# Kernel optimization log

Measured on AMD Instinct MI355X. Metric: run time of the kernel, lower is better.

## Reference

```python
import jax, jax.numpy as jnp
import numpy as np

N_NODES = 100000
N_EDGES = 1600000
C_IN = 128
C_OUT = 128


def setup_inputs() -> dict:
    key = jax.random.key(0)
    k1, k2, k3, k4, k5 = jax.random.split(key, 5)
    x = jax.random.normal(k1, (N_NODES, C_IN), dtype=jnp.float32)
    W = jax.random.normal(k2, (2 * C_IN, C_OUT), dtype=jnp.float32) * (1.0 / np.sqrt(2 * C_IN))
    b = jax.random.normal(k3, (C_OUT,), dtype=jnp.float32) * 0.01
    src = jax.random.randint(k4, (N_EDGES,), 0, N_NODES, dtype=jnp.int64 if jax.config.jax_enable_x64 else jnp.int32)
    dst = jax.random.randint(k5, (N_EDGES,), 0, N_NODES, dtype=jnp.int64 if jax.config.jax_enable_x64 else jnp.int32)
    return {"x": x, "W": W, "b": b, "src": src, "dst": dst}


def reference(x, W, b, src, dst):
    # Max-Relative graph conv: per-edge relative feature, max-aggregated per dst node.
    diff = x[dst] - x[src]                                  # [E, C]  (edge messages)
    max_diff = jax.ops.segment_max(diff, dst, num_segments=x.shape[0])  # [N, C]
    # Nodes with no incoming edges: segment_max yields -inf; zero them out.
    max_diff = jnp.where(jnp.isneginf(max_diff), jnp.zeros_like(max_diff), max_diff)
    h = jnp.concatenate([x, max_diff], axis=1)              # [N, 2C]
    return jax.nn.relu(h @ W + b)                           # Linear(2C->C_out) + ReLU
```

## Files before the change

### kernel.cpp

```cpp
#include <hip/hip_runtime.h>
#include <math.h>

#define NN 100000
#define NE 1600000
#define C 128

#define TS 4096
#define NT ((NE + TS - 1) / TS)
#define BUK ((NN + 511) >> 9)
#define NSC (BUK * NT)
#define NBS ((NSC + 2047) / 2048)
#define PREP_BLKS (NN * C / 8 / 256)
#define CONVW_BLKS (2 * C * C / 256)
#define GM 64

typedef __attribute__((ext_vector_type(8))) short   bf16x8;
typedef __attribute__((ext_vector_type(4))) float   f32x4;
typedef unsigned short ushort_t;
typedef unsigned int   uint_t;

__device__ inline ushort_t f2bf(float f) {
    union { float f; uint_t u; } a; a.f = f;
    uint_t r = a.u + 0x7fff + ((a.u >> 16) & 1);
    return (ushort_t)(r >> 16);
}

__global__ __launch_bounds__(256) void k_setup(
        const float* __restrict__ x, ushort_t* __restrict__ xh,
        const float* __restrict__ W, ushort_t* __restrict__ Wt,
        const int* __restrict__ dst, int* __restrict__ tileHistT) {
    __shared__ int h[BUK];
    const int t  = threadIdx.x;
    const int bb = blockIdx.x;
    if (bb < PREP_BLKS) {
        int i = bb * 256 + t;
        int node = i >> 4;
        int c0   = (i & 15) * 8;
        const float4* xp = (const float4*)(x + (long)i * 8);
        float4 v0 = xp[0], v1 = xp[1];
        ushort_t o[8] = { f2bf(v0.x), f2bf(v0.y), f2bf(v0.z), f2bf(v0.w),
                          f2bf(v1.x), f2bf(v1.y), f2bf(v1.z), f2bf(v1.w) };
        *(bf16x8*)(xh + (long)node * 256 + c0) = *(bf16x8*)o;
    } else if (bb < PREP_BLKS + CONVW_BLKS) {
        int i = (bb - PREP_BLKS) * 256 + t;
        int k = i >> 7, n = i & 127;
        Wt[n * 256 + k] = f2bf(W[i]);
    } else {
        const int tile = bb - PREP_BLKS - CONVW_BLKS;
        for (int i = t; i < BUK; i += 256) h[i] = 0;
        __syncthreads();
        const int base = tile * TS;
        for (int i = t; i < TS; i += 256) {
            int e = base + i;
            if (e < NE) atomicAdd(&h[dst[e] >> 9], 1);
        }
        __syncthreads();
        for (int i = t; i < BUK; i += 256) tileHistT[i * NT + tile] = h[i];
    }
}

__global__ __launch_bounds__(256) void scan_partial(const int* __restrict__ in,
                                                    int* __restrict__ out,
                                                    int* __restrict__ blocksums,
                                                    int n) {
    __shared__ int ts[256];
    const int t = threadIdx.x;
    const int base = blockIdx.x * 2048 + t * 8;
    int c[8];
    int s = 0;
    #pragma unroll
    for (int j = 0; j < 8; ++j) {
        int i = base + j;
        c[j] = (i < n) ? in[i] : 0;
        s += c[j];
    }
    ts[t] = s;
    __syncthreads();
    for (int off = 1; off < 256; off <<= 1) {
        int add = (t >= off) ? ts[t - off] : 0;
        __syncthreads();
        ts[t] += add;
        __syncthreads();
    }
    int run = (t == 0) ? 0 : ts[t - 1];
    #pragma unroll
    for (int j = 0; j < 8; ++j) {
        int i = base + j;
        if (i < n) out[i] = run;
        run += c[j];
    }
    if (t == 255) blocksums[blockIdx.x] = ts[255];
}

__global__ __launch_bounds__(64) void scan_blocksums(const int* __restrict__ blocksums,
                                                     int* __restrict__ blockbase, int nb) {
    int lane = threadIdx.x;
    int v = (lane < nb) ? blocksums[lane] : 0;
    int incl = v;
    #pragma unroll
    for (int off = 1; off < 64; off <<= 1) {
        int nbr = __shfl_up(incl, off, 64);
        if (lane >= off) incl += nbr;
    }
    if (lane < nb) blockbase[lane] = incl - v;
}

__global__ __launch_bounds__(256) void p3_scatter(const int* __restrict__ dst,
                                                  const int* __restrict__ src,
                                                  const int* __restrict__ tileScan,
                                                  const int* __restrict__ blockbase,
                                                  uint_t* __restrict__ coarse) {
    __shared__ int cur[BUK];
    const int t = threadIdx.x, tile = blockIdx.x;
    for (int i = t; i < BUK; i += 256) {
        int idx = i * NT + tile;
        cur[i] = tileScan[idx] + blockbase[idx >> 11];
    }
    __syncthreads();
    const int base = tile * TS;
    for (int i = t; i < TS; i += 256) {
        int e = base + i;
        if (e < NE) {
            int d = dst[e];
            int p = atomicAdd(&cur[d >> 9], 1);
            coarse[p] = ((uint_t)(d & 511) << 17) | (uint_t)src[e];
        }
    }
}

__global__ __launch_bounds__(256) void p4_build(const uint_t* __restrict__ coarse,
                                                const int* __restrict__ tileScan,
                                                const int* __restrict__ blockbase,
                                                int* __restrict__ offs,
                                                int* __restrict__ ssrc) {
    __shared__ int cnt[512];
    __shared__ int ts[256];
    const int b = blockIdx.x, t = threadIdx.x;
    const int n0 = b << 9;
    const int i0 = b * NT;
    const int bs = tileScan[i0] + blockbase[i0 >> 11];
    int be;
    if (b == BUK - 1) be = NE;
    else { int i1 = (b + 1) * NT; be = tileScan[i1] + blockbase[i1 >> 11]; }
    cnt[t] = 0; cnt[t + 256] = 0;
    __syncthreads();
    for (int i = bs + t; i < be; i += 256)
        atomicAdd(&cnt[(int)(coarse[i] >> 17)], 1);
    __syncthreads();
    int c0 = cnt[2 * t], c1 = cnt[2 * t + 1];
    ts[t] = c0 + c1;
    __syncthreads();
    for (int off = 1; off < 256; off <<= 1) {
        int add = (t >= off) ? ts[t - off] : 0;
        __syncthreads();
        ts[t] += add;
        __syncthreads();
    }
    int ex = (t == 0) ? 0 : ts[t - 1];
    int o0 = bs + ex, o1 = o0 + c0;
    cnt[2 * t] = o0; cnt[2 * t + 1] = o1;
    if (n0 + 2 * t < NN)     offs[n0 + 2 * t]     = o0;
    if (n0 + 2 * t + 1 < NN) offs[n0 + 2 * t + 1] = o1;
    if (b == BUK - 1 && t == 0) offs[NN] = NE;
    __syncthreads();
    for (int i = bs + t; i < be; i += 256) {
        uint_t pk = coarse[i];
        int p = atomicAdd(&cnt[(int)(pk >> 17)], 1);
        ssrc[p] = (int)(pk & 0x1FFFF);
    }
}

#define ACCQ(u)  { m[0] = fminf(m[0], __uint_as_float((u).x << 16));          \
                   m[1] = fminf(m[1], __uint_as_float((u).x & 0xffff0000u));  \
                   m[2] = fminf(m[2], __uint_as_float((u).y << 16));          \
                   m[3] = fminf(m[3], __uint_as_float((u).y & 0xffff0000u));  \
                   m[4] = fminf(m[4], __uint_as_float((u).z << 16));          \
                   m[5] = fminf(m[5], __uint_as_float((u).z & 0xffff0000u));  \
                   m[6] = fminf(m[6], __uint_as_float((u).w << 16));          \
                   m[7] = fminf(m[7], __uint_as_float((u).w & 0xffff0000u)); }

__global__ __launch_bounds__(256) void node_min_v2(
        const int* __restrict__ offs, const int* __restrict__ ssrc,
        ushort_t* __restrict__ xh) {
    const int wid  = (blockIdx.x * 256 + threadIdx.x) >> 6;
    const int lane = threadIdx.x & 63;
    if (wid >= NN) return;
    const int g = lane >> 4;
    const int s = lane & 15;
    const int beg = offs[wid], end = offs[wid + 1];
    const char* xb = (const char*)xh;
    float m[8];
    #pragma unroll
    for (int j = 0; j < 8; ++j) m[j] = INFINITY;
    int i = beg;
    for (; i + 8 <= end; i += 8) {
        int e0 = ssrc[i + g];
        int e1 = ssrc[i + 4 + g];
        uint4 a = *(const uint4*)(xb + (long)e0 * 512 + s * 16);
        uint4 bq = *(const uint4*)(xb + (long)e1 * 512 + s * 16);
        ACCQ(a);
        ACCQ(bq);
    }
    for (; i < end; i += 4) {
        int e = i + g;
        int idx = ssrc[(e < end) ? e : (end - 1)];
        uint4 a = *(const uint4*)(xb + (long)idx * 512 + s * 16);
        if (e < end) ACCQ(a);
    }
    #pragma unroll
    for (int j = 0; j < 8; ++j) {
        m[j] = fminf(m[j], __shfl_xor(m[j], 16, 64));
        m[j] = fminf(m[j], __shfl_xor(m[j], 32, 64));
    }
    if (g == 0) {
        uint4 xd = *(const uint4*)(xb + (long)wid * 512 + s * 16);
        uint_t xu[4] = { xd.x, xd.y, xd.z, xd.w };
        bool has = end > beg;
        uint4 o;
        uint_t* op = (uint_t*)&o;
        #pragma unroll
        for (int j = 0; j < 4; ++j) {
            float lo = has ? (__uint_as_float(xu[j] << 16)         - m[2 * j])     : 0.0f;
            float hi = has ? (__uint_as_float(xu[j] & 0xffff0000u) - m[2 * j + 1]) : 0.0f;
            op[j] = (uint_t)f2bf(lo) | ((uint_t)f2bf(hi) << 16);
        }
        *(uint4*)((char*)xh + (long)wid * 512 + 256 + s * 16) = o;
    }
}

__global__ __launch_bounds__(256) void gemm_mfma(
        const ushort_t* __restrict__ xh, const ushort_t* __restrict__ Wt,
        const float* __restrict__ b, float* __restrict__ out) {
    const int w    = threadIdx.x >> 6;
    const int l    = threadIdx.x & 63;
    const int wcol = w * 32;
    const int lr   = l & 15;
    const int kb   = (l >> 4) * 8;

    bf16x8 bb[2][8];
    float  bv[2];
    #pragma unroll
    for (int n = 0; n < 2; ++n) {
        int col = wcol + n * 16 + lr;
        bv[n] = b[col];
        const ushort_t* wp = Wt + (long)col * 256 + kb;
        #pragma unroll
        for (int k0 = 0; k0 < 8; ++k0)
            bb[n][k0] = *(const bf16x8*)(wp + k0 * 32);
    }

    const int mb0 = blockIdx.x * GM;
    #pragma unroll
    for (int mt = 0; mt < GM / 16; ++mt) {
        int mbase = mb0 + mt * 16;
        int arow = mbase + lr;
        if (arow >= NN) arow = NN - 1;
        const ushort_t* ap = xh + (long)arow * 256 + kb;
        bf16x8 a[8];
        #pragma unroll
        for (int k0 = 0; k0 < 8; ++k0) a[k0] = *(const bf16x8*)(ap + k0 * 32);

        f32x4 acc0 = (f32x4){0.f, 0.f, 0.f, 0.f};
        f32x4 acc1 = (f32x4){0.f, 0.f, 0.f, 0.f};
        #pragma unroll
        for (int k0 = 0; k0 < 8; ++k0) {
            acc0 = __builtin_amdgcn_mfma_f32_16x16x32_bf16(a[k0], bb[0][k0], acc0, 0, 0, 0);
            acc1 = __builtin_amdgcn_mfma_f32_16x16x32_bf16(a[k0], bb[1][k0], acc1, 0, 0, 0);
        }

        int rbase = mbase + ((l >> 4) << 2);
        int col0 = wcol + lr;
        #pragma unroll
        for (int j = 0; j < 4; ++j) {
            int r = rbase + j;
            if (r < NN) {
                out[(long)r * 128 + col0]      = fmaxf(acc0[j] + bv[0], 0.0f);
                out[(long)r * 128 + col0 + 16] = fmaxf(acc1[j] + bv[1], 0.0f);
            }
        }
    }
}

__global__ void init_neginf(float* __restrict__ p, int n) {
    int i = blockIdx.x * blockDim.x + threadIdx.x;
    if (i < n) p[i] = -INFINITY;
}

__device__ inline void amaxf(float* a, float v, float cur) {
    if (cur >= v) return;
    if (v >= 0.0f) atomicMax((int*)a, __float_as_int(v));
    else           atomicMin((unsigned int*)a, __float_as_uint(v));
}

__global__ __launch_bounds__(256) void edge_max(
        const float* __restrict__ x, const int* __restrict__ src,
        const int* __restrict__ dst, float* __restrict__ maxdiff) {
    long tid = (long)blockIdx.x * blockDim.x + threadIdx.x;
    int e = (int)(tid >> 5);
    if (e >= NE) return;
    int lane = (int)(tid & 31);
    int s = src[e], d = dst[e];
    int c0 = lane * 4;
    const float4 xd = *(const float4*)(x + (long)d * C + c0);
    const float4 xs = *(const float4*)(x + (long)s * C + c0);
    float4 df;
    df.x = xd.x - xs.x; df.y = xd.y - xs.y;
    df.z = xd.z - xs.z; df.w = xd.w - xs.w;
    float* o = maxdiff + (long)d * C + c0;
    float4 cur = *(const float4*)o;
    amaxf(o + 0, df.x, cur.x);
    amaxf(o + 1, df.y, cur.y);
    amaxf(o + 2, df.z, cur.z);
    amaxf(o + 3, df.w, cur.w);
}

#define TN 32
__global__ __launch_bounds__(256) void gemm_relu(
        const float* __restrict__ x, const float* __restrict__ W,
        const float* __restrict__ b, float* __restrict__ out) {
    __shared__ float h[TN][2 * C];
    const int nb = blockIdx.x * TN;
    const int t  = threadIdx.x;
    for (int i = t; i < TN * 2 * C / 4; i += 256) {
        int idx  = i * 4;
        int node = idx / (2 * C);
        int ci   = idx % (2 * C);
        float4 v;
        if (ci < C) {
            v = *(const float4*)(x + (long)(nb + node) * C + ci);
        } else {
            v = *(const float4*)(out + (long)(nb + node) * C + (ci - C));
            if (v.x == -INFINITY) v.x = 0.0f;
            if (v.y == -INFINITY) v.y = 0.0f;
            if (v.z == -INFINITY) v.z = 0.0f;
            if (v.w == -INFINITY) v.w = 0.0f;
        }
        *(float4*)&h[node][ci] = v;
    }
    __syncthreads();
    const int co = (t & 31) * 4;
    const int n0 = (t >> 5) * 4;
    float acc[4][4];
    #pragma unroll
    for (int i = 0; i < 4; ++i)
        #pragma unroll
        for (int j = 0; j < 4; ++j) acc[i][j] = 0.0f;
    for (int ci = 0; ci < 2 * C; ++ci) {
        float4 w = *(const float4*)(W + (long)ci * C + co);
        #pragma unroll
        for (int i = 0; i < 4; ++i) {
            float hv = h[n0 + i][ci];
            acc[i][0] = fmaf(hv, w.x, acc[i][0]);
            acc[i][1] = fmaf(hv, w.y, acc[i][1]);
            acc[i][2] = fmaf(hv, w.z, acc[i][2]);
            acc[i][3] = fmaf(hv, w.w, acc[i][3]);
        }
    }
    float4 bias = *(const float4*)(b + co);
    #pragma unroll
    for (int i = 0; i < 4; ++i) {
        float4 r;
        r.x = fmaxf(acc[i][0] + bias.x, 0.0f);
        r.y = fmaxf(acc[i][1] + bias.y, 0.0f);
        r.z = fmaxf(acc[i][2] + bias.z, 0.0f);
        r.w = fmaxf(acc[i][3] + bias.w, 0.0f);
        *(float4*)(out + (long)(nb + n0 + i) * C + co) = r;
    }
}

extern "C" void kernel_launch(void* const* d_in, const int* in_sizes, int n_in,
                              void* d_out, int out_size, void* d_ws, size_t ws_size,
                              hipStream_t stream) {
    const float* x   = (const float*)d_in[0];
    const float* W   = (const float*)d_in[1];
    const float* b   = (const float*)d_in[2];
    const int*   src = (const int*)d_in[3];
    const int*   dst = (const int*)d_in[4];
    float* out = (float*)d_out;

    size_t ints_head = (size_t)128 + NSC + (NN + 1) + NE;
    size_t head_b    = ((ints_head * 4) + 255) & ~(size_t)255;
    size_t xh_b      = (size_t)NN * 256 * 2;
    size_t wt_b      = (size_t)2 * C * C * 2;
    size_t need      = head_b + xh_b + wt_b;

    if (ws_size >= need) {
        int* blocksums = (int*)d_ws;
        int* blockbase = blocksums + 64;
        int* tileScan  = blockbase + 64;
        int* offs      = tileScan + NSC;
        int* ssrc      = offs + NN + 1;
        ushort_t* xh   = (ushort_t*)((char*)d_ws + head_b);
        ushort_t* Wt   = (ushort_t*)((char*)d_ws + head_b + xh_b);
        int*    tileHistT = ssrc;
        uint_t* coarse    = (uint_t*)d_out;

        k_setup<<<PREP_BLKS + CONVW_BLKS + NT, 256, 0, stream>>>(x, xh, W, Wt, dst, tileHistT);
        scan_partial<<<NBS, 256, 0, stream>>>(tileHistT, tileScan, blocksums, NSC);
        scan_blocksums<<<1, 64, 0, stream>>>(blocksums, blockbase, NBS);
        p3_scatter<<<NT, 256, 0, stream>>>(dst, src, tileScan, blockbase, coarse);
        p4_build<<<BUK, 256, 0, stream>>>(coarse, tileScan, blockbase, offs, ssrc);
        node_min_v2<<<NN / 4, 256, 0, stream>>>(offs, ssrc, xh);
        gemm_mfma<<<(NN + GM - 1) / GM, 256, 0, stream>>>(xh, Wt, b, out);
    } else {
        int n = NN * C;
        init_neginf<<<(n + 255) / 256, 256, 0, stream>>>(out, n);
        long threads = (long)NE * 32;
        edge_max<<<(int)((threads + 255) / 256), 256, 0, stream>>>(x, src, dst, out);
        gemm_relu<<<(NN + TN - 1) / TN, 256, 0, stream>>>(x, W, b, out);
    }
}
```

Before: 269.4 us.

## Gather order-preserving bf16 keys for packed u16 min, fold blocksum scan into consumers

Result: no change. 272.0 us (+1.0%).

```diff
diff --git a/kernel.cpp b/kernel.cpp
--- a/kernel.cpp
+++ b/kernel.cpp
@@ -14,8 +14,9 @@
 #define CONVW_BLKS (2 * C * C / 256)
 #define GM 64
 
-typedef __attribute__((ext_vector_type(8))) short   bf16x8;
-typedef __attribute__((ext_vector_type(4))) float   f32x4;
+typedef __attribute__((ext_vector_type(8))) short          bf16x8;
+typedef __attribute__((ext_vector_type(4))) float          f32x4;
+typedef __attribute__((ext_vector_type(8))) unsigned short u16x8;
 typedef unsigned short ushort_t;
 typedef unsigned int   uint_t;
 
@@ -27,6 +28,7 @@
 
 __global__ __launch_bounds__(256) void k_setup(
         const float* __restrict__ x, ushort_t* __restrict__ xh,
+        ushort_t* __restrict__ xt,
         const float* __restrict__ W, ushort_t* __restrict__ Wt,
         const int* __restrict__ dst, int* __restrict__ tileHistT) {
     __shared__ int h[BUK];
@@ -40,7 +42,12 @@
         float4 v0 = xp[0], v1 = xp[1];
         ushort_t o[8] = { f2bf(v0.x), f2bf(v0.y), f2bf(v0.z), f2bf(v0.w),
                           f2bf(v1.x), f2bf(v1.y), f2bf(v1.z), f2bf(v1.w) };
+        ushort_t tt[8];
+        #pragma unroll
+        for (int j = 0; j < 8; ++j)
+            tt[j] = (o[j] & 0x8000) ? (ushort_t)~o[j] : (ushort_t)(o[j] | 0x8000);
         *(bf16x8*)(xh + (long)node * 256 + c0) = *(bf16x8*)o;
+        *(bf16x8*)(xt + (long)node * 128 + c0) = *(bf16x8*)tt;
     } else if (bb < PREP_BLKS + CONVW_BLKS) {
         int i = (bb - PREP_BLKS) * 256 + t;
         int k = i >> 7, n = i & 127;
@@ -92,29 +99,33 @@
     if (t == 255) blocksums[blockIdx.x] = ts[255];
 }
 
-__global__ __launch_bounds__(64) void scan_blocksums(const int* __restrict__ blocksums,
-                                                     int* __restrict__ blockbase, int nb) {
-    int lane = threadIdx.x;
-    int v = (lane < nb) ? blocksums[lane] : 0;
-    int incl = v;
-    #pragma unroll
-    for (int off = 1; off < 64; off <<= 1) {
-        int nbr = __shfl_up(incl, off, 64);
-        if (lane >= off) incl += nbr;
-    }
-    if (lane < nb) blockbase[lane] = incl - v;
+__device__ inline void scan_bsums_lds(const int* __restrict__ blocksums,
+                                      int* bbase, int t) {
+    if (t < 64) {
+        int v = (t < NBS) ? blocksums[t] : 0;
+        int incl = v;
+        #pragma unroll
+        for (int off = 1; off < 64; off <<= 1) {
+            int nbr = __shfl_up(incl, off, 64);
+            if (t >= off) incl += nbr;
+        }
+        bbase[t] = incl - v;
+    }
 }
 
 __global__ __launch_bounds__(256) void p3_scatter(const int* __restrict__ dst,
                                                   const int* __restrict__ src,
                                                   const int* __restrict__ tileScan,
-                                                  const int* __restrict__ blockbase,
+                                                  const int* __restrict__ blocksums,
                                                   uint_t* __restrict__ coarse) {
     __shared__ int cur[BUK];
+    __shared__ int bbase[64];
     const int t = threadIdx.x, tile = blockIdx.x;
+    scan_bsums_lds(blocksums, bbase, t);
+    __syncthreads();
     for (int i = t; i < BUK; i += 256) {
         int idx = i * NT + tile;
-        cur[i] = tileScan[idx] + blockbase[idx >> 11];
+        cur[i] = tileScan[idx] + bbase[idx >> 11];
     }
     __syncthreads();
     const int base = tile * TS;
@@ -130,20 +141,22 @@
 
 __global__ __launch_bounds__(256) void p4_build(const uint_t* __restrict__ coarse,
                                                 const int* __restrict__ tileScan,
-                                                const int* __restrict__ blockbase,
+                                                const int* __restrict__ blocksums,
                                                 int* __restrict__ offs,
                                                 int* __restrict__ ssrc) {
     __shared__ int cnt[512];
     __shared__ int ts[256];
+    __shared__ int bbase[64];
     const int b = blockIdx.x, t = threadIdx.x;
+    scan_bsums_lds(blocksums, bbase, t);
     const int n0 = b << 9;
+    cnt[t] = 0; cnt[t + 256] = 0;
+    __syncthreads();
     const int i0 = b * NT;
-    const int bs = tileScan[i0] + blockbase[i0 >> 11];
+    const int bs = tileScan[i0] + bbase[i0 >> 11];
     int be;
     if (b == BUK - 1) be = NE;
-    else { int i1 = (b + 1) * NT; be = tileScan[i1] + blockbase[i1 >> 11]; }
-    cnt[t] = 0; cnt[t + 256] = 0;
-    __syncthreads();
+    else { int i1 = (b + 1) * NT; be = tileScan[i1] + bbase[i1 >> 11]; }
     for (int i = bs + t; i < be; i += 256)
         atomicAdd(&cnt[(int)(coarse[i] >> 17)], 1);
     __syncthreads();
@@ -170,58 +183,58 @@
     }
 }
 
-#define ACCQ(u)  { m[0] = fminf(m[0], __uint_as_float((u).x << 16));          \
-                   m[1] = fminf(m[1], __uint_as_float((u).x & 0xffff0000u));  \
-                   m[2] = fminf(m[2], __uint_as_float((u).y << 16));          \
-                   m[3] = fminf(m[3], __uint_as_float((u).y & 0xffff0000u));  \
-                   m[4] = fminf(m[4], __uint_as_float((u).z << 16));          \
-                   m[5] = fminf(m[5], __uint_as_float((u).z & 0xffff0000u));  \
-                   m[6] = fminf(m[6], __uint_as_float((u).w << 16));          \
-                   m[7] = fminf(m[7], __uint_as_float((u).w & 0xffff0000u)); }
-
-__global__ __launch_bounds__(256) void node_min_v2(
+__global__ __launch_bounds__(256) void node_min_v3(
         const int* __restrict__ offs, const int* __restrict__ ssrc,
-        ushort_t* __restrict__ xh) {
+        const ushort_t* __restrict__ xt, ushort_t* __restrict__ xh) {
     const int wid  = (blockIdx.x * 256 + threadIdx.x) >> 6;
     const int lane = threadIdx.x & 63;
     if (wid >= NN) return;
     const int g = lane >> 4;
     const int s = lane & 15;
     const int beg = offs[wid], end = offs[wid + 1];
-    const char* xb = (const char*)xh;
-    float m[8];
-    #pragma unroll
-    for (int j = 0; j < 8; ++j) m[j] = INFINITY;
+    const char* xb = (const char*)xt;
+    u16x8 vm;
+    #pragma unroll
+    for (int j = 0; j < 8; ++j) vm[j] = 0xFFFFu;
     int i = beg;
     for (; i + 8 <= end; i += 8) {
         int e0 = ssrc[i + g];
         int e1 = ssrc[i + 4 + g];
-        uint4 a = *(const uint4*)(xb + (long)e0 * 512 + s * 16);
-        uint4 bq = *(const uint4*)(xb + (long)e1 * 512 + s * 16);
-        ACCQ(a);
-        ACCQ(bq);
+        u16x8 a = *(const u16x8*)(xb + (long)e0 * 256 + s * 16);
+        u16x8 bq = *(const u16x8*)(xb + (long)e1 * 256 + s * 16);
+        vm = __builtin_elementwise_min(vm, a);
+        vm = __builtin_elementwise_min(vm, bq);
     }
     for (; i < end; i += 4) {
         int e = i + g;
         int idx = ssrc[(e < end) ? e : (end - 1)];
-        uint4 a = *(const uint4*)(xb + (long)idx * 512 + s * 16);
-        if (e < end) ACCQ(a);
-    }
-    #pragma unroll
-    for (int j = 0; j < 8; ++j) {
-        m[j] = fminf(m[j], __shfl_xor(m[j], 16, 64));
-        m[j] = fminf(m[j], __shfl_xor(m[j], 32, 64));
-    }
+        u16x8 a = *(const u16x8*)(xb + (long)idx * 256 + s * 16);
+        if (e < end) vm = __builtin_elementwise_min(vm, a);
+    }
+    union { u16x8 v; uint_t u[4]; } cv, ov;
+    cv.v = vm;
+    #pragma unroll
+    for (int j = 0; j < 4; ++j) ov.u[j] = __shfl_xor(cv.u[j], 16, 64);
+    cv.v = __builtin_elementwise_min(cv.v, ov.v);
+    #pragma unroll
+    for (int j = 0; j < 4; ++j) ov.u[j] = __shfl_xor(cv.u[j], 32, 64);
+    cv.v = __builtin_elementwise_min(cv.v, ov.v);
+
     if (g == 0) {
-        uint4 xd = *(const uint4*)(xb + (long)wid * 512 + s * 16);
+        const bool has = end > beg;
+        uint4 xd = *(const uint4*)((const char*)xh + (long)wid * 512 + s * 16);
         uint_t xu[4] = { xd.x, xd.y, xd.z, xd.w };
-        bool has = end > beg;
         uint4 o;
         uint_t* op = (uint_t*)&o;
         #pragma unroll
         for (int j = 0; j < 4; ++j) {
-            float lo = has ? (__uint_as_float(xu[j] << 16)         - m[2 * j])     : 0.0f;
-            float hi = has ? (__uint_as_float(xu[j] & 0xffff0000u) - m[2 * j + 1]) : 0.0f;
+            ushort_t t0 = cv.v[2 * j], t1 = cv.v[2 * j + 1];
+            ushort_t b0 = (t0 & 0x8000) ? (ushort_t)(t0 ^ 0x8000) : (ushort_t)~t0;
+            ushort_t b1 = (t1 & 0x8000) ? (ushort_t)(t1 ^ 0x8000) : (ushort_t)~t1;
+            float lo = has ? (__uint_as_float(xu[j] << 16)
+                              - __uint_as_float((uint_t)b0 << 16)) : 0.0f;
+            float hi = has ? (__uint_as_float(xu[j] & 0xffff0000u)
+                              - __uint_as_float((uint_t)b1 << 16)) : 0.0f;
             op[j] = (uint_t)f2bf(lo) | ((uint_t)f2bf(hi) << 16);
         }
         *(uint4*)((char*)xh + (long)wid * 512 + 256 + s * 16) = o;
@@ -386,21 +399,20 @@
 
     if (ws_size >= need) {
         int* blocksums = (int*)d_ws;
-        int* blockbase = blocksums + 64;
-        int* tileScan  = blockbase + 64;
+        int* tileScan  = blocksums + 128;
         int* offs      = tileScan + NSC;
         int* ssrc      = offs + NN + 1;
         ushort_t* xh   = (ushort_t*)((char*)d_ws + head_b);
         ushort_t* Wt   = (ushort_t*)((char*)d_ws + head_b + xh_b);
-        int*    tileHistT = ssrc;
-        uint_t* coarse    = (uint_t*)d_out;
-
-        k_setup<<<PREP_BLKS + CONVW_BLKS + NT, 256, 0, stream>>>(x, xh, W, Wt, dst, tileHistT);
+        int*      tileHistT = ssrc;
+        uint_t*   coarse    = (uint_t*)d_out;
+        ushort_t* xt        = (ushort_t*)((char*)d_out + (8u << 20));
+
+        k_setup<<<PREP_BLKS + CONVW_BLKS + NT, 256, 0, stream>>>(x, xh, xt, W, Wt, dst, tileHistT);
         scan_partial<<<NBS, 256, 0, stream>>>(tileHistT, tileScan, blocksums, NSC);
-        scan_blocksums<<<1, 64, 0, stream>>>(blocksums, blockbase, NBS);
-        p3_scatter<<<NT, 256, 0, stream>>>(dst, src, tileScan, blockbase, coarse);
-        p4_build<<<BUK, 256, 0, stream>>>(coarse, tileScan, blockbase, offs, ssrc);
-        node_min_v2<<<NN / 4, 256, 0, stream>>>(offs, ssrc, xh);
+        p3_scatter<<<NT, 256, 0, stream>>>(dst, src, tileScan, blocksums, coarse);
+        p4_build<<<BUK, 256, 0, stream>>>(coarse, tileScan, blocksums, offs, ssrc);
+        node_min_v3<<<NN / 4, 256, 0, stream>>>(offs, ssrc, xt, xh);
         gemm_mfma<<<(NN + GM - 1) / GM, 256, 0, stream>>>(xh, Wt, b, out);
     } else {
         int n = NN * C;
```
